# Performance work log

Hardware: AMD Instinct MI355X
Metric: run time of the kernel (lower is better)

The kernel has to match this reference:

```python
import jax, jax.numpy as jnp
import numpy as np

N = 100000   # total nodes across the batch
D = 3        # ambient dimension of the point cloud
T = 64       # num_thetas (directions)
R = 64       # resolution of the ECT discretization
B = 128      # number of point clouds in the batch
RADIUS = 1.1
SCALE = 8.0


def setup_inputs() -> dict:
    key = jax.random.key(0)
    kx, kv, kb = jax.random.split(key, 3)
    x = jax.random.normal(kx, (N, D), dtype=jnp.float32)
    # directions; the layer stores v movedim'd and moves it back, so math uses [D, T]
    v = jax.random.normal(kv, (D, T), dtype=jnp.float32)
    v = v / jnp.linalg.norm(v, axis=0, keepdims=True)  # unit directions, typical usage
    batch = jnp.sort(jax.random.randint(kb, (N,), 0, B, dtype=jnp.int64))
    return {"x": x, "v": v, "batch": batch}


def reference(x, v, batch):
    # compute_ect_points:
    # nh[n,t] = <x_n, v_t>
    nh = x @ v  # [N, T]
    lin = jnp.linspace(-RADIUS, RADIUS, R, dtype=x.dtype)  # [R]
    # ecc[n,t,r] = sigmoid(scale * (lin[r] - nh[n,t]))  -- large [N,T,R] intermediate
    ecc = jax.nn.sigmoid(SCALE * (lin[None, None, :] - nh[:, :, None]))
    # scatter-sum over the batch index (index_add): -> [B, T, R]
    ect = jax.ops.segment_sum(ecc, batch, num_segments=B)
    # normalized=False -> return ect.squeeze(); no singleton dims here
    return ect
```

## Files before the change

### kernel.cpp

```cpp
#include <hip/hip_runtime.h>
#include <math.h>


#define THREADS 256
#define TPB 4
#define TQ  16
#define ROWLEN 225
#define PAD 63
#define STEPS 148

#if __has_builtin(__builtin_amdgcn_exp2f)
#define EXP2F(x) __builtin_amdgcn_exp2f(x)
#else
#define EXP2F(x) exp2f(x)
#endif
#if __has_builtin(__builtin_amdgcn_rcpf)
#define RCPF(x) __builtin_amdgcn_rcpf(x)
#else
#define RCPF(x) (1.0f / (x))
#endif

constexpr double cexp_taylor(double r) {
    double s = 1.0, term = 1.0;
    for (int i = 1; i < 18; ++i) { term *= r / (double)i; s += term; }
    return s;
}
constexpr double cexp(double x) {
    const double LN2 = 0.69314718055994530942;
    const int n = (int)(x / LN2 + (x >= 0.0 ? 0.5 : -0.5));
    const double r = x - (double)n * LN2;
    double e = cexp_taylor(r);
    if (n >= 0) { for (int i = 0; i < n;  ++i) e *= 2.0; }
    else        { for (int i = 0; i < -n; ++i) e *= 0.5; }
    return e;
}
struct WTab {
    float w[STEPS];
    constexpr WTab() : w() {
        const double d = 2.2 / 63.0;
        for (int j = 0; j < STEPS; ++j) {
            const double z = 8.0 * d * (double)(111 - j);
            w[j] = (float)(1.0 / ((1.0 + cexp(-z)) * 65536.0));
        }
    }
};
constexpr WTab WT;

__device__ __forceinline__ int lb64(const int* __restrict__ A, int n, int val,
                                    int lane) {
    int lo = 0, hi = n;
    while (hi - lo > 64) {
        const long long span = hi - lo;
        const int p = lo + (int)((span * lane) >> 6);
        const unsigned long long m = __ballot(A[p] < val);
        const int c = __popcll(m);
        if (c == 0) { hi = lo; break; }
        const int plast = lo + (int)((span * (c - 1)) >> 6);
        const int pnext = (c < 64) ? (lo + (int)((span * (long long)c) >> 6)) : hi;
        lo = plast + 1; hi = pnext;
    }
    const int span = hi - lo;
    const unsigned long long m = __ballot(lane < span && A[lo + lane] < val);
    return lo + __popcll(m);
}

__global__ __launch_bounds__(THREADS, 8) void ect_fused5_kernel(
    const float* __restrict__ x,
    const float* __restrict__ v,
    const int*   __restrict__ batch,
    float* __restrict__ out,
    int n, float inv_d, float bias)
{
    __shared__ unsigned HistU[TPB][ROWLEN];
    float* HistF = (float*)&HistU[0][0];

    const int tid  = threadIdx.x;
    const int wv   = tid >> 6;
    const int lane = tid & 63;
    const int b    = blockIdx.x >> 4;
    const int tq   = blockIdx.x & (TQ - 1);

    {
        unsigned* hz = &HistU[0][0];
        for (int i = tid; i < TPB * ROWLEN; i += THREADS) hz[i] = 0u;
    }

    const int s0 = lb64(batch, n, b, lane);
    const int s1 = lb64(batch, n, b + 1, lane);

    const int t_l  = lane >> 4;
    const int slot = (lane & 15) + (wv << 4);
    const int tbase = tq * TPB;
    const int t    = tbase + t_l;
    const float va = v[t], vb = v[64 + t], vc = v[128 + t];

    __syncthreads();

    for (int base = s0; base < s1; base += 64) {
        const int idx = base + slot;
        if (idx < s1) {
            const float3 xx = *(const float3*)(x + 3 * (size_t)idx);
            const float nh = fmaf(xx.x, va, fmaf(xx.y, vb, xx.z * vc));
            float bin = fmaf(nh, inv_d, bias);
            bin = fminf(fmaxf(bin, 0.0f), 158.999f);
            const float g0f = floorf(bin);
            const float fr  = bin - g0f;
            const int   g0  = (int)g0f;
            const unsigned q1 = (unsigned)(fr * 65536.0f + 0.5f);
            const unsigned q0 = 65536u - q1;
            atomicAdd(&HistU[t_l][PAD + g0],     q0);
            atomicAdd(&HistU[t_l][PAD + g0 + 1], q1);
        }
    }

    __syncthreads();

    {
        unsigned* hu = &HistU[0][0];
        for (int i = tid; i < TPB * ROWLEN; i += THREADS)
            HistF[i] = (float)hu[i];
    }

    __syncthreads();

    const float* H = HistF + wv * ROWLEN + lane;
    float a0 = 0.f, a1 = 0.f;
#pragma unroll
    for (int j = 0; j < STEPS; j += 2) {
        a0 = fmaf(WT.w[j],     H[j],     a0);
        a1 = fmaf(WT.w[j + 1], H[j + 1], a1);
    }
    out[((size_t)b * 64 + tbase + wv) * 64 + lane] = a0 + a1;
}

extern "C" void kernel_launch(void* const* d_in, const int* in_sizes, int n_in,
                              void* d_out, int out_size, void* d_ws, size_t ws_size,
                              hipStream_t stream) {
    const float* x     = (const float*)d_in[0];
    const float* v     = (const float*)d_in[1];
    const int*   batch = (const int*)d_in[2];
    float*       out   = (float*)d_out;

    const int n = in_sizes[0] / 3;

    const double d = 2.2 / 63.0;
    const float inv_d = (float)(1.0 / d);
    const float bias  = 79.5f;

    hipLaunchKernelGGL(ect_fused5_kernel, dim3(128 * TQ), dim3(THREADS), 0,
                       stream, x, v, batch, out, n, inv_d, bias);
}
```

Measured before the change: 17.32 us.

## Pack paired histogram updates into single 64-bit LDS atomics with even/odd split

Each point's two adjacent-bin contributions are packed into one 64-bit atomicAdd. The histogram is split into even-start and odd-start 64-bit word arrays, so an update at any bin alignment lands in a single word. A merge pass then adds the odd array, shifted by one, into the even array before the float conversion and the weighted reduction. The point loop also loads four points per thread before processing them, to raise memory-level parallelism. This halves the number of LDS atomics, at the cost of 64-bit atomics, twice the histogram memory and an extra merge step.

Result: no change. 17.52 us (+1.2%).

```diff
diff --git a/kernel.cpp b/kernel.cpp
--- a/kernel.cpp
+++ b/kernel.cpp
@@ -5,20 +5,11 @@
 #define THREADS 256
 #define TPB 4
 #define TQ  16
-#define ROWLEN 225
 #define PAD 63
 #define STEPS 148
-
-#if __has_builtin(__builtin_amdgcn_exp2f)
-#define EXP2F(x) __builtin_amdgcn_exp2f(x)
-#else
-#define EXP2F(x) exp2f(x)
-#endif
-#if __has_builtin(__builtin_amdgcn_rcpf)
-#define RCPF(x) __builtin_amdgcn_rcpf(x)
-#else
-#define RCPF(x) (1.0f / (x))
-#endif
+#define ROW32 228
+#define ROW64 114
+#define HO_BASE64 (TPB * ROW64)
 
 constexpr double cexp_taylor(double r) {
     double s = 1.0, term = 1.0;
@@ -64,15 +55,14 @@
     return lo + __popcll(m);
 }
 
-__global__ __launch_bounds__(THREADS, 8) void ect_fused5_kernel(
+__global__ __launch_bounds__(THREADS, 8) void ect_fused6_kernel(
     const float* __restrict__ x,
     const float* __restrict__ v,
     const int*   __restrict__ batch,
     float* __restrict__ out,
     int n, float inv_d, float bias)
 {
-    __shared__ unsigned HistU[TPB][ROWLEN];
-    float* HistF = (float*)&HistU[0][0];
+    __shared__ unsigned long long Hu[2 * TPB * ROW64];
 
     const int tid  = threadIdx.x;
     const int wv   = tid >> 6;
@@ -80,10 +70,7 @@
     const int b    = blockIdx.x >> 4;
     const int tq   = blockIdx.x & (TQ - 1);
 
-    {
-        unsigned* hz = &HistU[0][0];
-        for (int i = tid; i < TPB * ROWLEN; i += THREADS) hz[i] = 0u;
-    }
+    for (int i = tid; i < 2 * TPB * ROW64; i += THREADS) Hu[i] = 0ull;
 
     const int s0 = lb64(batch, n, b, lane);
     const int s1 = lb64(batch, n, b + 1, lane);
@@ -93,37 +80,59 @@
     const int tbase = tq * TPB;
     const int t    = tbase + t_l;
     const float va = v[t], vb = v[64 + t], vc = v[128 + t];
+    const int rowoff64 = t_l * ROW64;
 
     __syncthreads();
 
-    for (int base = s0; base < s1; base += 64) {
-        const int idx = base + slot;
-        if (idx < s1) {
-            const float3 xx = *(const float3*)(x + 3 * (size_t)idx);
-            const float nh = fmaf(xx.x, va, fmaf(xx.y, vb, xx.z * vc));
+    for (int base = s0; base < s1; base += 4 * 64) {
+        float xs0[4], xs1[4], xs2[4];
+        bool  ok[4];
+#pragma unroll
+        for (int k = 0; k < 4; ++k) {
+            const int idx = base + (k << 6) + slot;
+            ok[k] = (idx < s1);
+            if (ok[k]) {
+                const float3 xx = *(const float3*)(x + 3 * (size_t)idx);
+                xs0[k] = xx.x; xs1[k] = xx.y; xs2[k] = xx.z;
+            }
+        }
+#pragma unroll
+        for (int k = 0; k < 4; ++k) {
+            if (!ok[k]) continue;
+            const float nh = fmaf(xs0[k], va, fmaf(xs1[k], vb, xs2[k] * vc));
             float bin = fmaf(nh, inv_d, bias);
             bin = fminf(fmaxf(bin, 0.0f), 158.999f);
             const float g0f = floorf(bin);
             const float fr  = bin - g0f;
-            const int   g0  = (int)g0f;
+            const int   a   = PAD + (int)g0f;
             const unsigned q1 = (unsigned)(fr * 65536.0f + 0.5f);
             const unsigned q0 = 65536u - q1;
-            atomicAdd(&HistU[t_l][PAD + g0],     q0);
-            atomicAdd(&HistU[t_l][PAD + g0 + 1], q1);
+            const unsigned long long val =
+                (unsigned long long)q0 | ((unsigned long long)q1 << 32);
+            const int w64 = (a >> 1) + rowoff64 + ((a & 1) ? HO_BASE64 : 0);
+            atomicAdd(&Hu[w64], val);
         }
     }
 
     __syncthreads();
 
     {
-        unsigned* hu = &HistU[0][0];
-        for (int i = tid; i < TPB * ROWLEN; i += THREADS)
-            HistF[i] = (float)hu[i];
+        unsigned* He32 = (unsigned*)Hu;
+        unsigned* Ho32 = (unsigned*)(Hu + HO_BASE64);
+        if (tid < ROW32) {
+#pragma unroll
+            for (int tt = 0; tt < TPB; ++tt) {
+                const int i = tt * ROW32 + tid;
+                unsigned s = He32[i];
+                if (tid > 0) s += Ho32[i - 1];
+                ((float*)He32)[i] = (float)s;
+            }
+        }
     }
 
     __syncthreads();
 
-    const float* H = HistF + wv * ROWLEN + lane;
+    const float* H = (const float*)Hu + wv * ROW32 + lane;
     float a0 = 0.f, a1 = 0.f;
 #pragma unroll
     for (int j = 0; j < STEPS; j += 2) {
@@ -147,6 +156,6 @@
     const float inv_d = (float)(1.0 / d);
     const float bias  = 79.5f;
 
-    hipLaunchKernelGGL(ect_fused5_kernel, dim3(128 * TQ), dim3(THREADS), 0,
+    hipLaunchKernelGGL(ect_fused6_kernel, dim3(128 * TQ), dim3(THREADS), 0,
                        stream, x, v, batch, out, n, inv_d, bias);
 }
```
